# Performance work log

Hardware: AMD Instinct MI355X
Metric: run time of the kernel (lower is better)

The kernel has to match this reference:

```python
import jax, jax.numpy as jnp
import numpy as np

D_MODEL = 1024
NHEAD = 16
HEAD_DIM = D_MODEL // NHEAD
D_FF = 4096
BIAS_HID = 8
EPS = 1e-5


def _pair_bias(m, w1, b1, w2, b2):
    # m: [B,S,S] -> bias [B,S,S,nhead] via per-scalar MLP 1->hid->nhead
    h = jax.nn.relu(m[..., None] * w1 + b1)          # [B,S,S,hid]
    return jnp.einsum('bxyh,hn->bxyn', h, w2) + b2   # [B,S,S,nhead]


def _layernorm(x, g, b):
    mu = jnp.mean(x, axis=-1, keepdims=True)
    var = jnp.mean(jnp.square(x - mu), axis=-1, keepdims=True)
    return (x - mu) * jax.lax.rsqrt(var + EPS) * g + b


def setup_inputs() -> dict:
    key = jax.random.key(0)
    ks = jax.random.split(key, 20)
    B, S = 4, 1024
    sc = 1.0 / np.sqrt(D_MODEL)
    inp = {
        'src': jax.random.normal(ks[0], (B, S, D_MODEL), jnp.float32),
        't_deltas': jax.random.uniform(ks[1], (B, S, S), jnp.float32),
        'dists': jax.random.uniform(ks[2], (B, S, S), jnp.float32),
        'Wq': jax.random.normal(ks[3], (D_MODEL, D_MODEL), jnp.float32) * sc,
        'bq': jnp.zeros((D_MODEL,), jnp.float32),
        'Wk': jax.random.normal(ks[4], (D_MODEL, D_MODEL), jnp.float32) * sc,
        'bk': jnp.zeros((D_MODEL,), jnp.float32),
        'Wv': jax.random.normal(ks[5], (D_MODEL, D_MODEL), jnp.float32) * sc,
        'bv': jnp.zeros((D_MODEL,), jnp.float32),
        'tb_w1': jax.random.normal(ks[6], (BIAS_HID,), jnp.float32),
        'tb_b1': jnp.zeros((BIAS_HID,), jnp.float32),
        'tb_w2': jax.random.normal(ks[7], (BIAS_HID, NHEAD), jnp.float32) * 0.3,
        'tb_b2': jnp.zeros((NHEAD,), jnp.float32),
        'db_w1': jax.random.normal(ks[8], (BIAS_HID,), jnp.float32),
        'db_b1': jnp.zeros((BIAS_HID,), jnp.float32),
        'db_w2': jax.random.normal(ks[9], (BIAS_HID, NHEAD), jnp.float32) * 0.3,
        'db_b2': jnp.zeros((NHEAD,), jnp.float32),
        'W1': jax.random.normal(ks[10], (D_MODEL, D_FF), jnp.float32) * sc,
        'b1': jnp.zeros((D_FF,), jnp.float32),
        'W2': jax.random.normal(ks[11], (D_FF, D_MODEL), jnp.float32) / np.sqrt(D_FF),
        'b2': jnp.zeros((D_MODEL,), jnp.float32),
        'g1': jnp.ones((D_MODEL,), jnp.float32),
        'beta1': jnp.zeros((D_MODEL,), jnp.float32),
        'g2': jnp.ones((D_MODEL,), jnp.float32),
        'beta2': jnp.zeros((D_MODEL,), jnp.float32),
    }
    return inp


def reference(src, t_deltas, dists, Wq, bq, Wk, bk, Wv, bv,
              tb_w1, tb_b1, tb_w2, tb_b2, db_w1, db_b1, db_w2, db_b2,
              W1, b1, W2, b2, g1, beta1, g2, beta2):
    B, S, _ = src.shape
    # QKV projections -> [B, H, S, hd]
    q = (src @ Wq + bq).reshape(B, S, NHEAD, HEAD_DIM).transpose(0, 2, 1, 3)
    k = (src @ Wk + bk).reshape(B, S, NHEAD, HEAD_DIM).transpose(0, 2, 1, 3)
    v = (src @ Wv + bv).reshape(B, S, NHEAD, HEAD_DIM).transpose(0, 2, 1, 3)
    # scores scaled by sqrt(d_model) (as in the original, not head_dim)
    scores = jnp.einsum('bhqd,bhkd->bhqk', q, k) / jnp.sqrt(jnp.float32(D_MODEL))
    bias = (_pair_bias(t_deltas, tb_w1, tb_b1, tb_w2, tb_b2)
            + _pair_bias(dists, db_w1, db_b1, db_w2, db_b2))  # [B,S,S,H]
    scores = scores + bias.transpose(0, 3, 1, 2)
    attn = jax.nn.softmax(scores, axis=-1)
    out = jnp.einsum('bhqk,bhkd->bhqd', attn, v)
    out = out.transpose(0, 2, 1, 3).reshape(B, S, D_MODEL)
    x = _layernorm(src + out, g1, beta1)
    ffn = jax.nn.relu(x @ W1 + b1) @ W2 + b2
    return _layernorm(x + ffn, g2, beta2)
```

## Files before the change

### kernel.cpp

```cpp
#include <hip/hip_runtime.h>

typedef __bf16 bf16x8 __attribute__((ext_vector_type(8)));
typedef float f32x4 __attribute__((ext_vector_type(4)));
typedef unsigned short u16;

__device__ __forceinline__ u16 f2bf(float f) {
  union { float f; unsigned u; } x; x.f = f;
  unsigned r = x.u + 0x7fffu + ((x.u >> 16) & 1u);
  return (u16)(r >> 16);
}
__device__ __forceinline__ float bf2f(u16 u) {
  union { unsigned u; float f; } x; x.u = ((unsigned)u) << 16;
  return x.f;
}
__device__ __forceinline__ void gl_lds16(const void* g, void* l) {
  __builtin_amdgcn_global_load_lds(
      (const __attribute__((address_space(1))) void*)g,
      (__attribute__((address_space(3))) void*)l, 16, 0, 0);
}

__global__ __launch_bounds__(256) void cvt_kernel(const float* __restrict__ in,
                                                  u16* __restrict__ out, int n4) {
  int i = blockIdx.x * 256 + threadIdx.x;
  if (i >= n4) return;
  float4 v = ((const float4*)in)[i];
  unsigned lo = (unsigned)f2bf(v.x) | ((unsigned)f2bf(v.y) << 16);
  unsigned hi = (unsigned)f2bf(v.z) | ((unsigned)f2bf(v.w) << 16);
  uint2 u; u.x = lo; u.y = hi;
  *(uint2*)&out[(size_t)i * 4] = u;
}

__global__ __launch_bounds__(256) void tconv_kernel(const float* __restrict__ in,
                                                    u16* __restrict__ out, int R, int C) {
  __shared__ float tile[32][33];
  int c0 = blockIdx.x * 32, r0 = blockIdx.y * 32;
  int tx = threadIdx.x & 31, ty = threadIdx.x >> 5;
#pragma unroll
  for (int i = 0; i < 4; i++)
    tile[ty + i * 8][tx] = in[(size_t)(r0 + ty + i * 8) * C + c0 + tx];
  __syncthreads();
#pragma unroll
  for (int i = 0; i < 4; i++)
    out[(size_t)(c0 + ty + i * 8) * R + r0 + tx] = f2bf(tile[tx][ty + i * 8]);
}

__global__ __launch_bounds__(256) void bcat_kernel(const float* __restrict__ bq,
                                                   const float* __restrict__ bk,
                                                   const float* __restrict__ bv,
                                                   float* __restrict__ o) {
  int i = blockIdx.x * 256 + threadIdx.x;
  if (i >= 3072) return;
  o[i] = i < 1024 ? bq[i] : (i < 2048 ? bk[i - 1024] : bv[i - 2048]);
}

#define BM 128
#define BN 128
#define BKG 32

template <int EPI>
__global__ __launch_bounds__(256) void gemm_kernel(const u16* __restrict__ A,
                                                   const u16* __restrict__ Bt,
                                                   const float* __restrict__ bias,
                                                   void* __restrict__ out,
                                                   int M, int N, int K, float qscale,
                                                   int kslice) {
  __shared__ u16 As[BM * BKG];
  __shared__ u16 Bs[BN * BKG];
  int tid = threadIdx.x;
  int w = tid >> 6, l = tid & 63, l16 = l & 15, lhi = l >> 4;
  int m0 = blockIdx.y * BM, n0 = blockIdx.x * BN;
  int z = blockIdx.z;
  int kbeg = z * kslice, kend = kbeg + kslice;
  int mw = (w >> 1) * 64, nw = (w & 1) * 64;
  f32x4 acc[4][4] = {};

  int srow = w * 32 + (l >> 2);
  int scol = (l & 3) * 8;
  const u16* Ag = A + (size_t)(m0 + srow) * K + scol;
  const u16* Bg = Bt + (size_t)(n0 + srow) * K + scol;
  u16* AsW0 = &As[(w * 32) * BKG];
  u16* AsW1 = &As[(w * 32 + 16) * BKG];
  u16* BsW0 = &Bs[(w * 32) * BKG];
  u16* BsW1 = &Bs[(w * 32 + 16) * BKG];

  for (int k0 = kbeg; k0 < kend; k0 += BKG) {
    gl_lds16(Ag + k0, AsW0);
    gl_lds16(Ag + (size_t)16 * K + k0, AsW1);
    gl_lds16(Bg + k0, BsW0);
    gl_lds16(Bg + (size_t)16 * K + k0, BsW1);
    __syncthreads();
    bf16x8 af[4], bfr[4];
#pragma unroll
    for (int i = 0; i < 4; i++) {
      af[i] = *(const bf16x8*)&As[(mw + i * 16 + l16) * BKG + lhi * 8];
      bfr[i] = *(const bf16x8*)&Bs[(nw + i * 16 + l16) * BKG + lhi * 8];
    }
    __builtin_amdgcn_s_setprio(1);
#pragma unroll
    for (int mi = 0; mi < 4; mi++)
#pragma unroll
      for (int ni = 0; ni < 4; ni++)
        acc[mi][ni] = __builtin_amdgcn_mfma_f32_16x16x32_bf16(af[mi], bfr[ni], acc[mi][ni], 0, 0, 0);
    __builtin_amdgcn_s_setprio(0);
    __syncthreads();
  }

#pragma unroll
  for (int mi = 0; mi < 4; mi++) {
    int gr = m0 + mw + mi * 16 + lhi * 4;
#pragma unroll
    for (int ni = 0; ni < 4; ni++) {
      int gc = n0 + nw + ni * 16 + l16;
      float bv = (EPI == 0) ? ((z == 0 && bias) ? bias[gc] : 0.f) : bias[gc];
      if (EPI == 2) {
        int seg = gc >> 10, c = gc & 1023, h = c >> 6, d = c & 63;
        float sc = (seg == 0) ? qscale : 1.f;
#pragma unroll
        for (int r = 0; r < 4; r++) {
          int row = gr + r;
          int b = row >> 10, s = row & 1023;
          size_t idx = ((((size_t)seg * 4 + b) * 16 + h) * 1024 + s) * 64 + d;
          ((u16*)out)[idx] = f2bf((acc[mi][ni][r] + bv) * sc);
        }
      } else if (EPI == 1) {
#pragma unroll
        for (int r = 0; r < 4; r++) {
          float v = fmaxf(acc[mi][ni][r] + bv, 0.f);
          ((u16*)out)[(size_t)(gr + r) * N + gc] = f2bf(v);
        }
      } else {
#pragma unroll
        for (int r = 0; r < 4; r++)
          ((float*)out)[(size_t)z * M * N + (size_t)(gr + r) * N + gc] = acc[mi][ni][r] + bv;
      }
    }
  }
}

__global__ __launch_bounds__(256) void vtrans_kernel(const u16* __restrict__ v,
                                                     u16* __restrict__ vt) {
  __shared__ u16 t[64][72];
  int bh = blockIdx.y, s0 = blockIdx.x * 64;
  int tid = threadIdx.x;
  int r = tid >> 2, c = (tid & 3) * 16;
  const u16* src = v + ((size_t)bh * 1024 + s0 + r) * 64 + c;
  *(int4*)&t[r][c] = *(const int4*)src;
  *(int4*)&t[r][c + 8] = *(const int4*)(src + 8);
  __syncthreads();
  int d = tid >> 2, sc = (tid & 3) * 16;
  u16 tmp[16];
#pragma unroll
  for (int j = 0; j < 16; j++) tmp[j] = t[sc + j][d];
  u16* dst = vt + ((size_t)bh * 64 + d) * 1024 + s0 + sc;
  *(int4*)dst = *(int4*)&tmp[0];
  *(int4*)(dst + 8) = *(int4*)&tmp[8];
}

__global__ __launch_bounds__(256) void bias_kernel(
    const float* __restrict__ td, const float* __restrict__ dd,
    const float* __restrict__ tw1, const float* __restrict__ tb1,
    const float* __restrict__ tw2, const float* __restrict__ tb2,
    const float* __restrict__ dw1, const float* __restrict__ db1,
    const float* __restrict__ dw2, const float* __restrict__ db2,
    u16* __restrict__ biasout, int b0) {
  __shared__ float stw2[128], sdw2[128], sb2[16];
  __shared__ float stw1[8], stb1[8], sdw1[8], sdb1[8];
  int tid = threadIdx.x, x = blockIdx.x, bz = blockIdx.y;
  int b = b0 + bz;
  if (tid < 128) { stw2[tid] = tw2[tid]; sdw2[tid] = dw2[tid]; }
  if (tid < 16) sb2[tid] = tb2[tid] + db2[tid];
  if (tid < 8) { stw1[tid] = tw1[tid]; stb1[tid] = tb1[tid]; sdw1[tid] = dw1[tid]; sdb1[tid] = db1[tid]; }
  __syncthreads();
  float4 tv = ((const float4*)(td + ((size_t)b * 1024 + x) * 1024))[tid];
  float4 dv = ((const float4*)(dd + ((size_t)b * 1024 + x) * 1024))[tid];
  float tj[4] = {tv.x, tv.y, tv.z, tv.w};
  float dj[4] = {dv.x, dv.y, dv.z, dv.w};
  float ht[4][8], hd[4][8];
#pragma unroll
  for (int j = 0; j < 4; j++)
#pragma unroll
    for (int i = 0; i < 8; i++) {
      ht[j][i] = fmaxf(tj[j] * stw1[i] + stb1[i], 0.f);
      hd[j][i] = fmaxf(dj[j] * sdw1[i] + sdb1[i], 0.f);
    }
  u16* outb = biasout + (size_t)bz * 16 * 1024 * 1024 + (size_t)x * 1024 + tid * 4;
#pragma unroll
  for (int h = 0; h < 16; h++) {
    float a[4];
#pragma unroll
    for (int j = 0; j < 4; j++) {
      float s = sb2[h];
#pragma unroll
      for (int i = 0; i < 8; i++)
        s += ht[j][i] * stw2[i * 16 + h] + hd[j][i] * sdw2[i * 16 + h];
      a[j] = s;
    }
    unsigned lo = (unsigned)f2bf(a[0]) | ((unsigned)f2bf(a[1]) << 16);
    unsigned hi = (unsigned)f2bf(a[2]) | ((unsigned)f2bf(a[3]) << 16);
    uint2 u; u.x = lo; u.y = hi;
    *(uint2*)&outb[(size_t)h * 1024 * 1024] = u;
  }
}

#define LDA 72
__global__ __launch_bounds__(256) void attn_kernel(
    const u16* __restrict__ qg, const u16* __restrict__ kg, const u16* __restrict__ vtg,
    const u16* __restrict__ bias, float* __restrict__ attn_out, int b0) {
  __shared__ u16 Ks[64 * LDA];
  __shared__ u16 Vt[64 * LDA];
  __shared__ u16 Ps[64 * LDA];
  int tid = threadIdx.x;
  int w = tid >> 6, l = tid & 63, l16 = l & 15, lhi = l >> 4;
  int qt = blockIdx.x, h = blockIdx.y, bz = blockIdx.z;
  int b = b0 + bz;
  size_t bh = ((size_t)(b * 16 + h)) * 1024 * 64;
  const u16* biasb = bias + (size_t)bz * 16 * 1024 * 1024 + (size_t)h * 1024 * 1024;
  int qrow = qt * 64 + w * 16 + l16;
  bf16x8 qa[2];
  qa[0] = *(const bf16x8*)&qg[bh + (size_t)qrow * 64 + lhi * 8];
  qa[1] = *(const bf16x8*)&qg[bh + (size_t)qrow * 64 + 32 + lhi * 8];

  float m_run[4], l_run[4];
  f32x4 o[4] = {};
#pragma unroll
  for (int r = 0; r < 4; r++) { m_run[r] = -1e30f; l_run[r] = 0.f; }

  int kr0 = (tid * 2) >> 3, kc0 = ((tid * 2) & 7) * 8;
  int kr1 = (tid * 2 + 1) >> 3, kc1 = ((tid * 2 + 1) & 7) * 8;

  for (int kt = 0; kt < 16; kt++) {
    __syncthreads();
    *(int4*)&Ks[kr0 * LDA + kc0] = *(const int4*)&kg[bh + (size_t)(kt * 64 + kr0) * 64 + kc0];
    *(int4*)&Ks[kr1 * LDA + kc1] = *(const int4*)&kg[bh + (size_t)(kt * 64 + kr1) * 64 + kc1];
    *(int4*)&Vt[kr0 * LDA + kc0] = *(const int4*)&vtg[bh + (size_t)kr0 * 1024 + kt * 64 + kc0];
    *(int4*)&Vt[kr1 * LDA + kc1] = *(const int4*)&vtg[bh + (size_t)kr1 * 1024 + kt * 64 + kc1];
    __syncthreads();

    f32x4 s[4] = {};
    __builtin_amdgcn_s_setprio(1);
#pragma unroll
    for (int ni = 0; ni < 4; ni++)
#pragma unroll
      for (int ks = 0; ks < 2; ks++) {
        bf16x8 kb = *(const bf16x8*)&Ks[(ni * 16 + l16) * LDA + ks * 32 + lhi * 8];
        s[ni] = __builtin_amdgcn_mfma_f32_16x16x32_bf16(qa[ks], kb, s[ni], 0, 0, 0);
      }
    __builtin_amdgcn_s_setprio(0);
#pragma unroll
    for (int ni = 0; ni < 4; ni++)
#pragma unroll
      for (int r = 0; r < 4; r++) {
        int brow = qt * 64 + w * 16 + lhi * 4 + r;
        s[ni][r] += bf2f(biasb[(size_t)brow * 1024 + kt * 64 + ni * 16 + l16]);
      }
    float rs[4];
#pragma unroll
    for (int r = 0; r < 4; r++) {
      float m = fmaxf(fmaxf(s[0][r], s[1][r]), fmaxf(s[2][r], s[3][r]));
      m = fmaxf(m, __shfl_xor(m, 1, 16));
      m = fmaxf(m, __shfl_xor(m, 2, 16));
      m = fmaxf(m, __shfl_xor(m, 4, 16));
      m = fmaxf(m, __shfl_xor(m, 8, 16));
      float m2 = fmaxf(m_run[r], m);
      float sc = __expf(m_run[r] - m2);
      float sum = 0.f;
#pragma unroll
      for (int ni = 0; ni < 4; ni++) {
        float p = __expf(s[ni][r] - m2);
        s[ni][r] = p;
        sum += p;
      }
      sum += __shfl_xor(sum, 1, 16);
      sum += __shfl_xor(sum, 2, 16);
      sum += __shfl_xor(sum, 4, 16);
      sum += __shfl_xor(sum, 8, 16);
      l_run[r] = l_run[r] * sc + sum;
      m_run[r] = m2;
      rs[r] = sc;
    }
#pragma unroll
    for (int di = 0; di < 4; di++)
#pragma unroll
      for (int r = 0; r < 4; r++)
        o[di][r] *= rs[r];
#pragma unroll
    for (int ni = 0; ni < 4; ni++)
#pragma unroll
      for (int r = 0; r < 4; r++)
        Ps[(w * 16 + lhi * 4 + r) * LDA + ni * 16 + l16] = f2bf(s[ni][r]);
    __builtin_amdgcn_s_setprio(1);
#pragma unroll
    for (int ks = 0; ks < 2; ks++) {
      bf16x8 pa = *(const bf16x8*)&Ps[(w * 16 + l16) * LDA + ks * 32 + lhi * 8];
#pragma unroll
      for (int di = 0; di < 4; di++) {
        bf16x8 vb = *(const bf16x8*)&Vt[(di * 16 + l16) * LDA + ks * 32 + lhi * 8];
        o[di] = __builtin_amdgcn_mfma_f32_16x16x32_bf16(pa, vb, o[di], 0, 0, 0);
      }
    }
    __builtin_amdgcn_s_setprio(0);
  }
#pragma unroll
  for (int r = 0; r < 4; r++) {
    float inv = 1.f / l_run[r];
    int row = b * 1024 + qt * 64 + w * 16 + lhi * 4 + r;
#pragma unroll
    for (int di = 0; di < 4; di++)
      attn_out[(size_t)row * 1024 + h * 64 + di * 16 + l16] = o[di][r] * inv;
  }
}

template <int BF_OUT, int NRES>
__global__ __launch_bounds__(256) void ln_kernel(const float* __restrict__ a,
                                                 const float* __restrict__ r1,
                                                 const float* __restrict__ r2,
                                                 const float* __restrict__ g,
                                                 const float* __restrict__ beta,
                                                 float* __restrict__ outf,
                                                 u16* __restrict__ outbf) {
  int row = blockIdx.x, tid = threadIdx.x;
  __shared__ float red[8];
  float4 va = ((const float4*)(a + (size_t)row * 1024))[tid];
  float4 vr = ((const float4*)(r1 + (size_t)row * 1024))[tid];
  float v[4] = {va.x + vr.x, va.y + vr.y, va.z + vr.z, va.w + vr.w};
  if (NRES == 2) {
    float4 v2 = ((const float4*)(r2 + (size_t)row * 1024))[tid];
    v[0] += v2.x; v[1] += v2.y; v[2] += v2.z; v[3] += v2.w;
  }
  float s = v[0] + v[1] + v[2] + v[3];
#pragma unroll
  for (int off = 32; off >= 1; off >>= 1) s += __shfl_xor(s, off, 64);
  if ((tid & 63) == 0) red[tid >> 6] = s;
  __syncthreads();
  float mean = (red[0] + red[1] + red[2] + red[3]) * (1.f / 1024.f);
  float q = 0.f;
#pragma unroll
  for (int j = 0; j < 4; j++) { float d = v[j] - mean; q += d * d; }
#pragma unroll
  for (int off = 32; off >= 1; off >>= 1) q += __shfl_xor(q, off, 64);
  if ((tid & 63) == 0) red[4 + (tid >> 6)] = q;
  __syncthreads();
  float var = (red[4] + red[5] + red[6] + red[7]) * (1.f / 1024.f);
  float rstd = rsqrtf(var + 1e-5f);
  float4 gv = ((const float4*)g)[tid];
  float4 bv = ((const float4*)beta)[tid];
  float o0 = (v[0] - mean) * rstd * gv.x + bv.x;
  float o1 = (v[1] - mean) * rstd * gv.y + bv.y;
  float o2 = (v[2] - mean) * rstd * gv.z + bv.z;
  float o3 = (v[3] - mean) * rstd * gv.w + bv.w;
  float4 ov; ov.x = o0; ov.y = o1; ov.z = o2; ov.w = o3;
  ((float4*)(outf + (size_t)row * 1024))[tid] = ov;
  if (BF_OUT) {
    unsigned lo = (unsigned)f2bf(o0) | ((unsigned)f2bf(o1) << 16);
    unsigned hi = (unsigned)f2bf(o2) | ((unsigned)f2bf(o3) << 16);
    uint2 u; u.x = lo; u.y = hi;
    *(uint2*)&outbf[(size_t)row * 1024 + tid * 4] = u;
  }
}

extern "C" void kernel_launch(void* const* d_in, const int* in_sizes, int n_in,
                              void* d_out, int out_size, void* d_ws, size_t ws_size,
                              hipStream_t stream) {
  const float* src      = (const float*)d_in[0];
  const float* t_deltas = (const float*)d_in[1];
  const float* dists    = (const float*)d_in[2];
  const float* Wq = (const float*)d_in[3];
  const float* bq = (const float*)d_in[4];
  const float* Wk = (const float*)d_in[5];
  const float* bk = (const float*)d_in[6];
  const float* Wv = (const float*)d_in[7];
  const float* bv = (const float*)d_in[8];
  const float* tb_w1 = (const float*)d_in[9];
  const float* tb_b1 = (const float*)d_in[10];
  const float* tb_w2 = (const float*)d_in[11];
  const float* tb_b2 = (const float*)d_in[12];
  const float* db_w1 = (const float*)d_in[13];
  const float* db_b1 = (const float*)d_in[14];
  const float* db_w2 = (const float*)d_in[15];
  const float* db_b2 = (const float*)d_in[16];
  const float* W1 = (const float*)d_in[17];
  const float* b1 = (const float*)d_in[18];
  const float* W2 = (const float*)d_in[19];
  const float* b2 = (const float*)d_in[20];
  const float* g1 = (const float*)d_in[21];
  const float* beta1 = (const float*)d_in[22];
  const float* g2 = (const float*)d_in[23];
  const float* beta2 = (const float*)d_in[24];
  float* out = (float*)d_out;

  const size_t MB = 1024u * 1024;
  bool big = ws_size >= 160 * MB;
  int PB = big ? 2 : 1;
  int KSPLIT = big ? 2 : 1;

  char* ws = (char*)d_ws;
  size_t off = 0;
  auto alloc = [&](size_t n) { void* p = ws + off; off += (n + 255) & ~(size_t)255; return p; };
  u16* src_bf  = (u16*)alloc(4096u * 1024 * 2);
  u16* wqkv_bt = (u16*)alloc(3072u * 1024 * 2);
  u16* w1_bt   = (u16*)alloc(4096u * 1024 * 2);
  u16* w2_bt   = (u16*)alloc(1024u * 4096 * 2);
  float* bcat  = (float*)alloc(3072u * 4);
  u16* qkv     = (u16*)alloc(3u * 4 * 16 * 1024 * 64 * 2);
  u16* vt      = (u16*)alloc(4u * 16 * 64 * 1024 * 2);
  u16* slab    = (u16*)alloc((size_t)PB * 16 * 1024 * 1024 * 2);
  float* attn_out = (float*)alloc(4096u * 1024 * 4);
  (void)ws_size; (void)in_sizes; (void)n_in; (void)out_size;

  u16* q_bf = qkv;
  u16* k_bf = qkv + 4u * 16 * 1024 * 64;
  u16* v_bf = qkv + 8u * 16 * 1024 * 64;
  float* x_f32 = (float*)qkv;
  u16*   x_bf  = (u16*)((char*)qkv + 16 * MB);
  u16*   h_bf  = (u16*)vt;
  float* ffn0, * ffn1;
  if (big) {
    ffn0 = (float*)((char*)slab + 24 * MB);
    ffn1 = (float*)((char*)slab + 40 * MB);
  } else {
    ffn0 = attn_out;
    ffn1 = nullptr;
  }

  cvt_kernel<<<4096, 256, 0, stream>>>(src, src_bf, 4096 * 1024 / 4);
  tconv_kernel<<<dim3(32, 32), 256, 0, stream>>>(Wq, wqkv_bt, 1024, 1024);
  tconv_kernel<<<dim3(32, 32), 256, 0, stream>>>(Wk, wqkv_bt + 1024u * 1024, 1024, 1024);
  tconv_kernel<<<dim3(32, 32), 256, 0, stream>>>(Wv, wqkv_bt + 2048u * 1024, 1024, 1024);
  tconv_kernel<<<dim3(128, 32), 256, 0, stream>>>(W1, w1_bt, 1024, 4096);
  tconv_kernel<<<dim3(32, 128), 256, 0, stream>>>(W2, w2_bt, 4096, 1024);
  bcat_kernel<<<12, 256, 0, stream>>>(bq, bk, bv, bcat);

  gemm_kernel<2><<<dim3(24, 32, 1), 256, 0, stream>>>(src_bf, wqkv_bt, bcat, qkv,
                                                      4096, 3072, 1024, 1.f / 32.f, 1024);
  vtrans_kernel<<<dim3(16, 64), 256, 0, stream>>>(v_bf, vt);

  for (int p = 0; p < 4 / PB; p++) {
    bias_kernel<<<dim3(1024, PB), 256, 0, stream>>>(t_deltas, dists, tb_w1, tb_b1, tb_w2, tb_b2,
                                                    db_w1, db_b1, db_w2, db_b2, slab, p * PB);
    attn_kernel<<<dim3(16, 16, PB), 256, 0, stream>>>(q_bf, k_bf, vt, slab, attn_out, p * PB);
  }

  ln_kernel<1, 1><<<4096, 256, 0, stream>>>(src, attn_out, nullptr, g1, beta1, x_f32, x_bf);
  gemm_kernel<1><<<dim3(32, 32, 1), 256, 0, stream>>>(x_bf, w1_bt, b1, h_bf,
                                                      4096, 4096, 1024, 1.f, 1024);
  if (big) {
    gemm_kernel<0><<<dim3(8, 32, 2), 256, 0, stream>>>(h_bf, w2_bt, b2, ffn0,
                                                       4096, 1024, 4096, 1.f, 2048);
    ln_kernel<0, 2><<<4096, 256, 0, stream>>>(x_f32, ffn0, ffn1, g2, beta2, out, nullptr);
  } else {
    gemm_kernel<0><<<dim3(8, 32, 1), 256, 0, stream>>>(h_bf, w2_bt, b2, ffn0,
                                                       4096, 1024, 4096, 1.f, 4096);
    ln_kernel<0, 1><<<4096, 256, 0, stream>>>(x_f32, ffn0, nullptr, g2, beta2, out, nullptr);
  }
}
```

Before: 334.0 us.

## Replace GEMMs with 256x256 double-buffered swizzled tile kernel and bf16 split-K partials

Replaces the 128x128, BK=32 single-buffer GEMM with a 512-thread 256x256 tile kernel. It uses a 64-wide K step, XOR-swizzled LDS layout, two-stage global-to-LDS prefetch with explicit vmcnt waits, and a block-index swizzle for L2 locality. The FFN down-projection now uses 2 or 4 K-splits that write bf16 partials, which a new LN kernel sums. This cuts LDS and global traffic per FLOP and improves load/compute overlap. The cost is larger register and LDS use, fewer workgroups for the small-N GEMM, and reduced precision in the summed split-K partials.

```diff
diff --git a/kernel.cpp b/kernel.cpp
--- a/kernel.cpp
+++ b/kernel.cpp
@@ -53,65 +53,87 @@
   o[i] = i < 1024 ? bq[i] : (i < 2048 ? bk[i - 1024] : bv[i - 2048]);
 }
 
-#define BM 128
-#define BN 128
-#define BKG 32
+__device__ __forceinline__ void stage256(u16* ldsA, u16* ldsB,
+                                         const u16* Ag, const u16* Bg,
+                                         int K, int w, int lane) {
+  int r8 = lane >> 3;
+  int gcol = 8 * ((lane & 7) ^ r8);
+#pragma unroll
+  for (int c = 0; c < 4; c++) {
+    int r = c * 64 + w * 8 + r8;
+    gl_lds16(Ag + (size_t)r * K + gcol, ldsA + c * 4096 + w * 512);
+    gl_lds16(Bg + (size_t)r * K + gcol, ldsB + c * 4096 + w * 512);
+  }
+}
 
 template <int EPI>
-__global__ __launch_bounds__(256) void gemm_kernel(const u16* __restrict__ A,
-                                                   const u16* __restrict__ Bt,
-                                                   const float* __restrict__ bias,
-                                                   void* __restrict__ out,
-                                                   int M, int N, int K, float qscale,
-                                                   int kslice) {
-  __shared__ u16 As[BM * BKG];
-  __shared__ u16 Bs[BN * BKG];
-  int tid = threadIdx.x;
-  int w = tid >> 6, l = tid & 63, l16 = l & 15, lhi = l >> 4;
-  int m0 = blockIdx.y * BM, n0 = blockIdx.x * BN;
+__global__ __launch_bounds__(512, 2) void gemm256_kernel(const u16* __restrict__ A,
+                                                         const u16* __restrict__ Bt,
+                                                         const float* __restrict__ bias,
+                                                         void* __restrict__ out,
+                                                         int M, int N, int K,
+                                                         float qscale, int kslice) {
+  __shared__ u16 lds[2][2][16384];
+  int tid = threadIdx.x, w = tid >> 6, lane = tid & 63;
+  int l16 = lane & 15, lhi = lane >> 4;
+  int wr = w >> 2, wc = w & 3;
+  int GX = gridDim.x;
+  int nwg = GX * gridDim.y;
+  int nlin = blockIdx.y * GX + blockIdx.x;
+  int cpx = nwg >> 3;
+  int sw = (nlin & 7) * cpx + (nlin >> 3);
+  int m0 = (sw / GX) * 256, n0 = (sw % GX) * 256;
   int z = blockIdx.z;
-  int kbeg = z * kslice, kend = kbeg + kslice;
-  int mw = (w >> 1) * 64, nw = (w & 1) * 64;
-  f32x4 acc[4][4] = {};
-
-  int srow = w * 32 + (l >> 2);
-  int scol = (l & 3) * 8;
-  const u16* Ag = A + (size_t)(m0 + srow) * K + scol;
-  const u16* Bg = Bt + (size_t)(n0 + srow) * K + scol;
-  u16* AsW0 = &As[(w * 32) * BKG];
-  u16* AsW1 = &As[(w * 32 + 16) * BKG];
-  u16* BsW0 = &Bs[(w * 32) * BKG];
-  u16* BsW1 = &Bs[(w * 32 + 16) * BKG];
-
-  for (int k0 = kbeg; k0 < kend; k0 += BKG) {
-    gl_lds16(Ag + k0, AsW0);
-    gl_lds16(Ag + (size_t)16 * K + k0, AsW1);
-    gl_lds16(Bg + k0, BsW0);
-    gl_lds16(Bg + (size_t)16 * K + k0, BsW1);
-    __syncthreads();
-    bf16x8 af[4], bfr[4];
-#pragma unroll
-    for (int i = 0; i < 4; i++) {
-      af[i] = *(const bf16x8*)&As[(mw + i * 16 + l16) * BKG + lhi * 8];
-      bfr[i] = *(const bf16x8*)&Bs[(nw + i * 16 + l16) * BKG + lhi * 8];
-    }
-    __builtin_amdgcn_s_setprio(1);
-#pragma unroll
-    for (int mi = 0; mi < 4; mi++)
-#pragma unroll
-      for (int ni = 0; ni < 4; ni++)
-        acc[mi][ni] = __builtin_amdgcn_mfma_f32_16x16x32_bf16(af[mi], bfr[ni], acc[mi][ni], 0, 0, 0);
-    __builtin_amdgcn_s_setprio(0);
-    __syncthreads();
-  }
-
-#pragma unroll
-  for (int mi = 0; mi < 4; mi++) {
-    int gr = m0 + mw + mi * 16 + lhi * 4;
-#pragma unroll
-    for (int ni = 0; ni < 4; ni++) {
-      int gc = n0 + nw + ni * 16 + l16;
-      float bv = (EPI == 0) ? ((z == 0 && bias) ? bias[gc] : 0.f) : bias[gc];
+  int kbeg = z * kslice;
+  const u16* Ag = A + (size_t)m0 * K + kbeg;
+  const u16* Bg = Bt + (size_t)n0 * K + kbeg;
+  f32x4 acc[8][4] = {};
+  int colq0 = ((lhi) ^ (l16 & 7)) << 3;
+  int colq1 = ((4 | lhi) ^ (l16 & 7)) << 3;
+  int nt = kslice >> 6;
+
+  stage256(&lds[0][0][0], &lds[0][1][0], Ag, Bg, K, w, lane);
+  stage256(&lds[1][0][0], &lds[1][1][0], Ag + 64, Bg + 64, K, w, lane);
+
+  for (int t = 0; t < nt; ++t) {
+    if (t + 1 < nt) { asm volatile("s_waitcnt vmcnt(8)" ::: "memory"); }
+    else            { asm volatile("s_waitcnt vmcnt(0)" ::: "memory"); }
+    __builtin_amdgcn_s_barrier();
+    const u16* Ab = &lds[t & 1][0][0];
+    const u16* Bb = &lds[t & 1][1][0];
+#pragma unroll
+    for (int kk = 0; kk < 2; kk++) {
+      int cq = kk ? colq1 : colq0;
+      bf16x8 af[8], bfr[4];
+#pragma unroll
+      for (int m = 0; m < 8; m++)
+        af[m] = *(const bf16x8*)&Ab[(wr * 128 + m * 16 + l16) * 64 + cq];
+#pragma unroll
+      for (int nn = 0; nn < 4; nn++)
+        bfr[nn] = *(const bf16x8*)&Bb[(wc * 64 + nn * 16 + l16) * 64 + cq];
+      __builtin_amdgcn_s_setprio(1);
+#pragma unroll
+      for (int m = 0; m < 8; m++)
+#pragma unroll
+        for (int nn = 0; nn < 4; nn++)
+          acc[m][nn] = __builtin_amdgcn_mfma_f32_16x16x32_bf16(af[m], bfr[nn], acc[m][nn], 0, 0, 0);
+      __builtin_amdgcn_s_setprio(0);
+    }
+    __builtin_amdgcn_s_barrier();
+    if (t + 2 < nt)
+      stage256(&lds[t & 1][0][0], &lds[t & 1][1][0],
+               Ag + (t + 2) * 64, Bg + (t + 2) * 64, K, w, lane);
+  }
+
+#pragma unroll
+  for (int m = 0; m < 8; m++) {
+    int gr = m0 + wr * 128 + m * 16 + lhi * 4;
+#pragma unroll
+    for (int nn = 0; nn < 4; nn++) {
+      int gc = n0 + wc * 64 + nn * 16 + l16;
+      float bv;
+      if (EPI == 0 || EPI == 3) bv = (z == 0 && bias) ? bias[gc] : 0.f;
+      else bv = bias[gc];
       if (EPI == 2) {
         int seg = gc >> 10, c = gc & 1023, h = c >> 6, d = c & 63;
         float sc = (seg == 0) ? qscale : 1.f;
@@ -120,18 +142,20 @@
           int row = gr + r;
           int b = row >> 10, s = row & 1023;
           size_t idx = ((((size_t)seg * 4 + b) * 16 + h) * 1024 + s) * 64 + d;
-          ((u16*)out)[idx] = f2bf((acc[mi][ni][r] + bv) * sc);
+          ((u16*)out)[idx] = f2bf((acc[m][nn][r] + bv) * sc);
         }
       } else if (EPI == 1) {
 #pragma unroll
-        for (int r = 0; r < 4; r++) {
-          float v = fmaxf(acc[mi][ni][r] + bv, 0.f);
-          ((u16*)out)[(size_t)(gr + r) * N + gc] = f2bf(v);
-        }
+        for (int r = 0; r < 4; r++)
+          ((u16*)out)[(size_t)(gr + r) * N + gc] = f2bf(fmaxf(acc[m][nn][r] + bv, 0.f));
+      } else if (EPI == 3) {
+#pragma unroll
+        for (int r = 0; r < 4; r++)
+          ((u16*)out)[(size_t)z * M * N + (size_t)(gr + r) * N + gc] = f2bf(acc[m][nn][r] + bv);
       } else {
 #pragma unroll
         for (int r = 0; r < 4; r++)
-          ((float*)out)[(size_t)z * M * N + (size_t)(gr + r) * N + gc] = acc[mi][ni][r] + bv;
+          ((float*)out)[(size_t)z * M * N + (size_t)(gr + r) * N + gc] = acc[m][nn][r] + bv;
       }
     }
   }
@@ -310,10 +334,8 @@
   }
 }
 
-template <int BF_OUT, int NRES>
 __global__ __launch_bounds__(256) void ln_kernel(const float* __restrict__ a,
                                                  const float* __restrict__ r1,
-                                                 const float* __restrict__ r2,
                                                  const float* __restrict__ g,
                                                  const float* __restrict__ beta,
                                                  float* __restrict__ outf,
@@ -323,10 +345,6 @@
   float4 va = ((const float4*)(a + (size_t)row * 1024))[tid];
   float4 vr = ((const float4*)(r1 + (size_t)row * 1024))[tid];
   float v[4] = {va.x + vr.x, va.y + vr.y, va.z + vr.z, va.w + vr.w};
-  if (NRES == 2) {
-    float4 v2 = ((const float4*)(r2 + (size_t)row * 1024))[tid];
-    v[0] += v2.x; v[1] += v2.y; v[2] += v2.z; v[3] += v2.w;
-  }
   float s = v[0] + v[1] + v[2] + v[3];
 #pragma unroll
   for (int off = 32; off >= 1; off >>= 1) s += __shfl_xor(s, off, 64);
@@ -350,12 +368,49 @@
   float o3 = (v[3] - mean) * rstd * gv.w + bv.w;
   float4 ov; ov.x = o0; ov.y = o1; ov.z = o2; ov.w = o3;
   ((float4*)(outf + (size_t)row * 1024))[tid] = ov;
-  if (BF_OUT) {
-    unsigned lo = (unsigned)f2bf(o0) | ((unsigned)f2bf(o1) << 16);
-    unsigned hi = (unsigned)f2bf(o2) | ((unsigned)f2bf(o3) << 16);
-    uint2 u; u.x = lo; u.y = hi;
-    *(uint2*)&outbf[(size_t)row * 1024 + tid * 4] = u;
-  }
+  unsigned lo = (unsigned)f2bf(o0) | ((unsigned)f2bf(o1) << 16);
+  unsigned hi = (unsigned)f2bf(o2) | ((unsigned)f2bf(o3) << 16);
+  uint2 u; u.x = lo; u.y = hi;
+  *(uint2*)&outbf[(size_t)row * 1024 + tid * 4] = u;
+}
+
+__global__ __launch_bounds__(256) void ln2_kernel(const float* __restrict__ x,
+                                                  const u16* __restrict__ ff, int zs,
+                                                  const float* __restrict__ g,
+                                                  const float* __restrict__ beta,
+                                                  float* __restrict__ out) {
+  int row = blockIdx.x, tid = threadIdx.x;
+  __shared__ float red[8];
+  float4 xv = ((const float4*)(x + (size_t)row * 1024))[tid];
+  float v[4] = {xv.x, xv.y, xv.z, xv.w};
+  for (int z = 0; z < zs; z++) {
+    uint2 u = *(const uint2*)&ff[(size_t)z * 4096 * 1024 + (size_t)row * 1024 + tid * 4];
+    v[0] += bf2f(u.x & 0xffff); v[1] += bf2f(u.x >> 16);
+    v[2] += bf2f(u.y & 0xffff); v[3] += bf2f(u.y >> 16);
+  }
+  float s = v[0] + v[1] + v[2] + v[3];
+#pragma unroll
+  for (int off = 32; off >= 1; off >>= 1) s += __shfl_xor(s, off, 64);
+  if ((tid & 63) == 0) red[tid >> 6] = s;
+  __syncthreads();
+  float mean = (red[0] + red[1] + red[2] + red[3]) * (1.f / 1024.f);
+  float q = 0.f;
+#pragma unroll
+  for (int j = 0; j < 4; j++) { float d = v[j] - mean; q += d * d; }
+#pragma unroll
+  for (int off = 32; off >= 1; off >>= 1) q += __shfl_xor(q, off, 64);
+  if ((tid & 63) == 0) red[4 + (tid >> 6)] = q;
+  __syncthreads();
+  float var = (red[4] + red[5] + red[6] + red[7]) * (1.f / 1024.f);
+  float rstd = rsqrtf(var + 1e-5f);
+  float4 gv = ((const float4*)g)[tid];
+  float4 bv = ((const float4*)beta)[tid];
+  float4 ov;
+  ov.x = (v[0] - mean) * rstd * gv.x + bv.x;
+  ov.y = (v[1] - mean) * rstd * gv.y + bv.y;
+  ov.z = (v[2] - mean) * rstd * gv.z + bv.z;
+  ov.w = (v[3] - mean) * rstd * gv.w + bv.w;
+  ((float4*)(out + (size_t)row * 1024))[tid] = ov;
 }
 
 extern "C" void kernel_launch(void* const* d_in, const int* in_sizes, int n_in,
@@ -389,9 +444,9 @@
   float* out = (float*)d_out;
 
   const size_t MB = 1024u * 1024;
-  bool big = ws_size >= 160 * MB;
+  bool big = ws_size >= 150 * MB;
   int PB = big ? 2 : 1;
-  int KSPLIT = big ? 2 : 1;
+  int ZS = big ? 4 : 2;
 
   char* ws = (char*)d_ws;
   size_t off = 0;
@@ -405,7 +460,7 @@
   u16* vt      = (u16*)alloc(4u * 16 * 64 * 1024 * 2);
   u16* slab    = (u16*)alloc((size_t)PB * 16 * 1024 * 1024 * 2);
   float* attn_out = (float*)alloc(4096u * 1024 * 4);
-  (void)ws_size; (void)in_sizes; (void)n_in; (void)out_size;
+  (void)in_sizes; (void)n_in; (void)out_size;
 
   u16* q_bf = qkv;
   u16* k_bf = qkv + 4u * 16 * 1024 * 64;
@@ -413,14 +468,8 @@
   float* x_f32 = (float*)qkv;
   u16*   x_bf  = (u16*)((char*)qkv + 16 * MB);
   u16*   h_bf  = (u16*)vt;
-  float* ffn0, * ffn1;
-  if (big) {
-    ffn0 = (float*)((char*)slab + 24 * MB);
-    ffn1 = (float*)((char*)slab + 40 * MB);
-  } else {
-    ffn0 = attn_out;
-    ffn1 = nullptr;
-  }
+  u16*   ffnb  = big ? (u16*)((char*)slab + 24 * MB)
+                     : (u16*)attn_out;
 
   cvt_kernel<<<4096, 256, 0, stream>>>(src, src_bf, 4096 * 1024 / 4);
   tconv_kernel<<<dim3(32, 32), 256, 0, stream>>>(Wq, wqkv_bt, 1024, 1024);
@@ -430,8 +479,8 @@
   tconv_kernel<<<dim3(32, 128), 256, 0, stream>>>(W2, w2_bt, 4096, 1024);
   bcat_kernel<<<12, 256, 0, stream>>>(bq, bk, bv, bcat);
 
-  gemm_kernel<2><<<dim3(24, 32, 1), 256, 0, stream>>>(src_bf, wqkv_bt, bcat, qkv,
-                                                      4096, 3072, 1024, 1.f / 32.f, 1024);
+  gemm256_kernel<2><<<dim3(12, 16, 1), 512, 0, stream>>>(src_bf, wqkv_bt, bcat, qkv,
+                                                         4096, 3072, 1024, 1.f / 32.f, 1024);
   vtrans_kernel<<<dim3(16, 64), 256, 0, stream>>>(v_bf, vt);
 
   for (int p = 0; p < 4 / PB; p++) {
@@ -440,16 +489,10 @@
     attn_kernel<<<dim3(16, 16, PB), 256, 0, stream>>>(q_bf, k_bf, vt, slab, attn_out, p * PB);
   }
 
-  ln_kernel<1, 1><<<4096, 256, 0, stream>>>(src, attn_out, nullptr, g1, beta1, x_f32, x_bf);
-  gemm_kernel<1><<<dim3(32, 32, 1), 256, 0, stream>>>(x_bf, w1_bt, b1, h_bf,
-                                                      4096, 4096, 1024, 1.f, 1024);
-  if (big) {
-    gemm_kernel<0><<<dim3(8, 32, 2), 256, 0, stream>>>(h_bf, w2_bt, b2, ffn0,
-                                                       4096, 1024, 4096, 1.f, 2048);
-    ln_kernel<0, 2><<<4096, 256, 0, stream>>>(x_f32, ffn0, ffn1, g2, beta2, out, nullptr);
-  } else {
-    gemm_kernel<0><<<dim3(8, 32, 1), 256, 0, stream>>>(h_bf, w2_bt, b2, ffn0,
-                                                       4096, 1024, 4096, 1.f, 4096);
-    ln_kernel<0, 1><<<4096, 256, 0, stream>>>(x_f32, ffn0, nullptr, g2, beta2, out, nullptr);
-  }
-}
+  ln_kernel<<<4096, 256, 0, stream>>>(src, attn_out, g1, beta1, x_f32, x_bf);
+  gemm256_kernel<1><<<dim3(16, 16, 1), 512, 0, stream>>>(x_bf, w1_bt, b1, h_bf,
+                                                         4096, 4096, 1024, 1.f, 1024);
+  gemm256_kernel<3><<<dim3(4, 16, ZS), 512, 0, stream>>>(h_bf, w2_bt, b2, ffnb,
+                                                         4096, 1024, 4096, 1.f, 4096 / ZS);
+  ln2_kernel<<<4096, 256, 0, stream>>>(x_f32, ffnb, ZS, g2, beta2, out);
+}
```

Result: faster. 299.1 us (-10.4%).
